# Kernel tuning notes

Hardware: AMD Instinct MI355X
Metric: run time of the kernel (lower is better)

The kernel has to match this reference:

```python
import jax, jax.numpy as jnp
import numpy as np

NUM_HEADS = 16
HEAD_DIM = 256  # hidden_size // num_heads = 4096 // 16
SEQ = 240       # hardcoded in the original forward's view(1, 240, -1)
IN_SIZE = 4096
HID = 4096


def setup_inputs() -> dict:
    key = jax.random.key(0)
    ks = jax.random.split(key, 10)
    s = 0.02
    return {
        "input1": jax.random.normal(ks[0], (SEQ, IN_SIZE), jnp.float32),
        "input2": jax.random.normal(ks[1], (SEQ, IN_SIZE), jnp.float32),
        "Wq": jax.random.normal(ks[2], (HID, IN_SIZE), jnp.float32) * s,
        "bq": jax.random.normal(ks[3], (HID,), jnp.float32) * s,
        "Wk": jax.random.normal(ks[4], (HID, IN_SIZE), jnp.float32) * s,
        "bk": jax.random.normal(ks[5], (HID,), jnp.float32) * s,
        "Wv": jax.random.normal(ks[6], (HID, IN_SIZE), jnp.float32) * s,
        "bv": jax.random.normal(ks[7], (HID,), jnp.float32) * s,
    }


def reference(input1, input2, Wq, bq, Wk, bk, Wv, bv):
    # QKV projections (torch Linear: x @ W^T + b)
    q = input1 @ Wq.T + bq  # [S, HID]
    k = input2 @ Wk.T + bk
    v = input2 @ Wv.T + bv
    # [1, H, S, hd]
    q = q.reshape(1, SEQ, NUM_HEADS, HEAD_DIM).transpose(0, 2, 1, 3)
    k = k.reshape(1, SEQ, NUM_HEADS, HEAD_DIM).transpose(0, 2, 1, 3)
    v = v.reshape(1, SEQ, NUM_HEADS, HEAD_DIM).transpose(0, 2, 1, 3)
    scores = jnp.einsum("bhqd,bhkd->bhqk", q, k) / jnp.sqrt(jnp.float32(HEAD_DIM))
    w = jax.nn.softmax(scores, axis=-1)  # [1, H, Sq, Sk]
    # NOTE: the original does attention_weights.transpose(-2,-1) @ value, i.e. attn^T @ V
    out = jnp.einsum("bhqk,bhqd->bhkd", w, v)  # [1, H, Sk, hd]
    out = out.transpose(0, 2, 1, 3).reshape(1, SEQ, HID)
    # linear_out exists in __init__ but is never applied in forward.
    return out
```

## Files before the change

### kernel.cpp

```cpp
#include <hip/hip_runtime.h>
#include <hip/hip_bf16.h>

#define SEQ 240
#define HID 4096
#define NH 16
#define HD 256

typedef float f32x4 __attribute__((ext_vector_type(4)));
typedef short s16x8 __attribute__((ext_vector_type(8)));
typedef short s16x4 __attribute__((ext_vector_type(4)));

__device__ __forceinline__ short f2bf(float f) {
    unsigned u = __builtin_bit_cast(unsigned, f);
    unsigned r = u + 0x7FFFu + ((u >> 16) & 1u);
    return (short)(r >> 16);
}

__device__ __forceinline__ s16x8 cvt8(float4 a, float4 b) {
    s16x8 r;
    r[0] = f2bf(a.x); r[1] = f2bf(a.y); r[2] = f2bf(a.z); r[3] = f2bf(a.w);
    r[4] = f2bf(b.x); r[5] = f2bf(b.y); r[6] = f2bf(b.z); r[7] = f2bf(b.w);
    return r;
}

__device__ __forceinline__ s16x8 cvt8v(f32x4 a, f32x4 b) {
    s16x8 r;
    r[0] = f2bf(a[0]); r[1] = f2bf(a[1]); r[2] = f2bf(a[2]); r[3] = f2bf(a[3]);
    r[4] = f2bf(b[0]); r[5] = f2bf(b[1]); r[6] = f2bf(b[2]); r[7] = f2bf(b[3]);
    return r;
}

__device__ __forceinline__ void dma16(const void* g, void* l) {
    __builtin_amdgcn_global_load_lds(
        (const __attribute__((address_space(1))) unsigned int*)g,
        (__attribute__((address_space(3))) unsigned int*)l,
        16, 0, 0);
}

__global__ __launch_bounds__(256) void cvt_kernel(
    const float* __restrict__ in1, const float* __restrict__ in2,
    short* __restrict__ A1, short* __restrict__ A2)
{
    const int i = blockIdx.x * 256 + threadIdx.x;
    const float* __restrict__ src = blockIdx.y ? in2 : in1;
    short* __restrict__ dst = blockIdx.y ? A2 : A1;
    const int r = i >> 9;
    const int c = (i & 511) * 8;
    s16x8 v = (s16x8){0,0,0,0,0,0,0,0};
    if (r < SEQ) {
        float4 a = *(const float4*)&src[(size_t)r * HID + c];
        float4 b = *(const float4*)&src[(size_t)r * HID + c + 4];
        v = cvt8(a, b);
    }
    *(s16x8*)&dst[(size_t)r * HID + c] = v;
}

__global__ __launch_bounds__(256, 3) void qkv_gemm(
    const short* __restrict__ A1, const short* __restrict__ A2,
    const float* __restrict__ Wq, const float* __restrict__ Wk,
    const float* __restrict__ Wv,
    float* __restrict__ pqk, float* __restrict__ pvt, int KC)
{
    const int g  = blockIdx.y;
    const int z  = blockIdx.z;
    const int nb = blockIdx.x * 64;
    const short* __restrict__ A = (g == 0) ? A1 : A2;
    const float* __restrict__ W = (g == 0) ? Wq : (g == 1) ? Wk : Wv;

    const int tid  = threadIdx.x;
    const int lane = tid & 63;
    const int w    = tid >> 6;
    const int lr   = lane & 15;
    const int lg   = lane >> 4;

    __shared__ short As[2][256 * 32];
    __shared__ float Bs[2][64 * 32];

    f32x4 acc[4][4];
    #pragma unroll
    for (int m = 0; m < 4; ++m)
        #pragma unroll
        for (int n = 0; n < 4; ++n)
            acc[m][n] = (f32x4){0.f, 0.f, 0.f, 0.f};

    const short* gA[4];
    #pragma unroll
    for (int i = 0; i < 4; ++i) {
        const int row = (i * 4 + w) * 16 + (lane >> 2);
        const int c   = (lane & 3) ^ ((row >> 1) & 3);
        gA[i] = A + (size_t)row * HID + z * KC + c * 8;
    }
    const float* gW[2];
    #pragma unroll
    for (int i = 0; i < 2; ++i) {
        const int row = (i * 4 + w) * 8 + (lane >> 3);
        const int c   = (lane & 7) ^ (row & 7);
        gW[i] = W + (size_t)(nb + row) * HID + z * KC + c * 4;
    }

    int aoff[4];
    #pragma unroll
    for (int m = 0; m < 4; ++m) {
        const int row = w * 64 + m * 16 + lr;
        aoff[m] = row * 32 + ((lg ^ ((row >> 1) & 3)) * 8);
    }
    int boff0[4], boff1[4];
    #pragma unroll
    for (int n = 0; n < 4; ++n) {
        const int row = n * 16 + lr;
        boff0[n] = row * 32 + (((2 * lg)     ^ (row & 7)) * 4);
        boff1[n] = row * 32 + (((2 * lg + 1) ^ (row & 7)) * 4);
    }

    #pragma unroll
    for (int i = 0; i < 4; ++i) dma16(gA[i], &As[0][(i * 4 + w) * 512]);
    #pragma unroll
    for (int i = 0; i < 2; ++i) dma16(gW[i], &Bs[0][(i * 4 + w) * 256]);
    #pragma unroll
    for (int i = 0; i < 4; ++i) gA[i] += 32;
    #pragma unroll
    for (int i = 0; i < 2; ++i) gW[i] += 32;
    __syncthreads();

    const int NIT = KC / 32;
    for (int t = 0; t < NIT; ++t) {
        const int b = t & 1;
        if (t + 1 < NIT) {
            #pragma unroll
            for (int i = 0; i < 4; ++i) dma16(gA[i], &As[b ^ 1][(i * 4 + w) * 512]);
            #pragma unroll
            for (int i = 0; i < 2; ++i) dma16(gW[i], &Bs[b ^ 1][(i * 4 + w) * 256]);
            #pragma unroll
            for (int i = 0; i < 4; ++i) gA[i] += 32;
            #pragma unroll
            for (int i = 0; i < 2; ++i) gW[i] += 32;
        }

        s16x8 af[4], bf[4];
        #pragma unroll
        for (int m = 0; m < 4; ++m)
            af[m] = *(const s16x8*)&As[b][aoff[m]];
        #pragma unroll
        for (int n = 0; n < 4; ++n) {
            f32x4 x0 = *(const f32x4*)&Bs[b][boff0[n]];
            f32x4 x1 = *(const f32x4*)&Bs[b][boff1[n]];
            bf[n] = cvt8v(x0, x1);
        }
        #pragma unroll
        for (int m = 0; m < 4; ++m)
            #pragma unroll
            for (int n = 0; n < 4; ++n)
                acc[m][n] = __builtin_amdgcn_mfma_f32_16x16x32_bf16(af[m], bf[n], acc[m][n], 0, 0, 0);

        if (t + 1 < NIT) __syncthreads();
    }

    if (g == 2) {
        float* pout = pvt + (size_t)z * HID * SEQ;
        #pragma unroll
        for (int m = 0; m < 4; ++m) {
            const int row0 = w * 64 + m * 16 + lg * 4;
            if (row0 >= SEQ) continue;
            #pragma unroll
            for (int n = 0; n < 4; ++n) {
                const int col = nb + n * 16 + lr;
                float4 o = make_float4(acc[m][n][0], acc[m][n][1], acc[m][n][2], acc[m][n][3]);
                *(float4*)&pout[(size_t)col * SEQ + row0] = o;
            }
        }
    } else {
        float* pout = pqk + (size_t)(z * 2 + g) * SEQ * HID;
        #pragma unroll
        for (int m = 0; m < 4; ++m) {
            const int row0 = w * 64 + m * 16 + lg * 4;
            if (row0 >= SEQ) continue;
            #pragma unroll
            for (int n = 0; n < 4; ++n) {
                const int col = nb + n * 16 + lr;
                #pragma unroll
                for (int r = 0; r < 4; ++r)
                    pout[(size_t)(row0 + r) * HID + col] = acc[m][n][r];
            }
        }
    }
}

__global__ __launch_bounds__(256) void reduce_qk(
    const float* __restrict__ pqk,
    const float* __restrict__ bq, const float* __restrict__ bk,
    short* __restrict__ qb, short* __restrict__ kb, int KS)
{
    const int g   = blockIdx.y;
    const int idx = blockIdx.x * 256 + threadIdx.x;
    f32x4 s = (f32x4){0.f, 0.f, 0.f, 0.f};
    for (int z = 0; z < KS; ++z)
        s += *(const f32x4*)&pqk[(size_t)(z * 2 + g) * SEQ * HID + (size_t)idx * 4];
    const int n = (idx * 4) & (HID - 1);
    const float* bias = g ? bk : bq;
    s += *(const f32x4*)&bias[n];
    short* ob = g ? kb : qb;
    s16x4 o = (s16x4){f2bf(s[0]), f2bf(s[1]), f2bf(s[2]), f2bf(s[3])};
    *(s16x4*)&ob[(size_t)idx * 4] = o;
}

__global__ __launch_bounds__(256) void reduce_v(
    const float* __restrict__ pvt, const float* __restrict__ bv,
    short* __restrict__ vtb, int KS)
{
    const int idx = blockIdx.x * 256 + threadIdx.x;
    f32x4 s = (f32x4){0.f, 0.f, 0.f, 0.f};
    for (int z = 0; z < KS; ++z)
        s += *(const f32x4*)&pvt[(size_t)z * HID * SEQ + (size_t)idx * 4];
    const int n = idx / 60;
    const float b = bv[n];
    s16x4 o = (s16x4){f2bf(s[0] + b), f2bf(s[1] + b), f2bf(s[2] + b), f2bf(s[3] + b)};
    *(s16x4*)&vtb[(size_t)idx * 4] = o;
}

__global__ __launch_bounds__(256) void scores_kernel(
    const short* __restrict__ qb, const short* __restrict__ kb,
    short* __restrict__ ptb)
{
    const int it   = blockIdx.x;
    const int h    = blockIdx.y;
    const int tid  = threadIdx.x;
    const int lane = tid & 63;
    const int w    = tid >> 6;
    const int lr   = lane & 15;
    const int lg   = lane >> 4;
    const int jt0  = w * 4;
    const int NJT  = (w < 3) ? 4 : 3;

    __shared__ float redmax[4][16];
    __shared__ float redsum[4][16];

    f32x4 acc[4];
    #pragma unroll
    for (int j = 0; j < 4; ++j) acc[j] = (f32x4){0.f, 0.f, 0.f, 0.f};

    const int ib = it * 16;
    const short* qrow = &qb[(size_t)(ib + lr) * HID + h * HD + lg * 8];

    for (int d0 = 0; d0 < HD; d0 += 32) {
        s16x8 afr = *(const s16x8*)&qrow[d0];
        #pragma unroll
        for (int j = 0; j < 4; ++j) {
            if (j < NJT) {
                s16x8 bfr = *(const s16x8*)&kb[(size_t)((jt0 + j) * 16 + lr) * HID + h * HD + d0 + lg * 8];
                acc[j] = __builtin_amdgcn_mfma_f32_16x16x32_bf16(afr, bfr, acc[j], 0, 0, 0);
            }
        }
    }

    const float sc = 0.0625f;
    #pragma unroll
    for (int j = 0; j < 4; ++j) acc[j] *= sc;

    #pragma unroll
    for (int r = 0; r < 4; ++r) {
        float mx = -1e30f;
        #pragma unroll
        for (int j = 0; j < 4; ++j) if (j < NJT) mx = fmaxf(mx, acc[j][r]);
        #pragma unroll
        for (int s = 1; s < 16; s <<= 1) mx = fmaxf(mx, __shfl_xor(mx, s, 64));
        if (lr == 0) redmax[w][lg * 4 + r] = mx;
    }
    __syncthreads();
    #pragma unroll
    for (int r = 0; r < 4; ++r) {
        const int i = lg * 4 + r;
        float mx = fmaxf(fmaxf(redmax[0][i], redmax[1][i]),
                         fmaxf(redmax[2][i], redmax[3][i]));
        float sum = 0.f;
        #pragma unroll
        for (int j = 0; j < 4; ++j) {
            if (j < NJT) {
                float e = expf(acc[j][r] - mx);
                acc[j][r] = e;
                sum += e;
            }
        }
        #pragma unroll
        for (int s = 1; s < 16; s <<= 1) sum += __shfl_xor(sum, s, 64);
        if (lr == 0) redsum[w][i] = sum;
    }
    __syncthreads();
    #pragma unroll
    for (int r = 0; r < 4; ++r) {
        const int i = lg * 4 + r;
        const float inv = 1.f / (redsum[0][i] + redsum[1][i] + redsum[2][i] + redsum[3][i]);
        #pragma unroll
        for (int j = 0; j < 4; ++j) if (j < NJT) acc[j][r] *= inv;
    }
    #pragma unroll
    for (int j = 0; j < 4; ++j) {
        if (j < NJT) {
            const int jj = (jt0 + j) * 16 + lr;
            s16x4 o = (s16x4){f2bf(acc[j][0]), f2bf(acc[j][1]), f2bf(acc[j][2]), f2bf(acc[j][3])};
            *(s16x4*)&ptb[(size_t)(h * SEQ + jj) * SEQ + ib + lg * 4] = o;
        }
    }
}

__global__ __launch_bounds__(256) void pv_kernel(
    const short* __restrict__ ptb, const short* __restrict__ vtb,
    float* __restrict__ out)
{
    const int dt   = blockIdx.x;
    const int h    = blockIdx.y;
    const int tid  = threadIdx.x;
    const int lane = tid & 63;
    const int w    = tid >> 6;
    const int lr   = lane & 15;
    const int lg   = lane >> 4;
    const int NJT  = (w < 3) ? 4 : 3;

    f32x4 acc[4];
    #pragma unroll
    for (int j = 0; j < 4; ++j) acc[j] = (f32x4){0.f, 0.f, 0.f, 0.f};

    const short* vrow = &vtb[(size_t)(h * HD + dt * 16 + lr) * SEQ + lg * 8];

    for (int i0 = 0; i0 < 256; i0 += 32) {
        const bool ok = (i0 + lg * 8) < SEQ;
        s16x8 bfr = (s16x8){0,0,0,0,0,0,0,0};
        if (ok) bfr = *(const s16x8*)&vrow[i0];
        #pragma unroll
        for (int j = 0; j < 4; ++j) {
            if (j < NJT) {
                const int jt = w + j * 4;
                s16x8 afr = (s16x8){0,0,0,0,0,0,0,0};
                if (ok) afr = *(const s16x8*)&ptb[(size_t)(h * SEQ + jt * 16 + lr) * SEQ + i0 + lg * 8];
                acc[j] = __builtin_amdgcn_mfma_f32_16x16x32_bf16(afr, bfr, acc[j], 0, 0, 0);
            }
        }
    }

    #pragma unroll
    for (int j = 0; j < 4; ++j) {
        if (j < NJT) {
            const int jt = w + j * 4;
            #pragma unroll
            for (int r = 0; r < 4; ++r)
                out[(size_t)(jt * 16 + lg * 4 + r) * HID + h * HD + dt * 16 + lr] = acc[j][r];
        }
    }
}

extern "C" void kernel_launch(void* const* d_in, const int* in_sizes, int n_in,
                              void* d_out, int out_size, void* d_ws, size_t ws_size,
                              hipStream_t stream) {
    const float* in1 = (const float*)d_in[0];
    const float* in2 = (const float*)d_in[1];
    const float* Wq  = (const float*)d_in[2];
    const float* bq  = (const float*)d_in[3];
    const float* Wk  = (const float*)d_in[4];
    const float* bk  = (const float*)d_in[5];
    const float* Wv  = (const float*)d_in[6];
    const float* bv  = (const float*)d_in[7];
    float* out = (float*)d_out;

    char* w = (char*)d_ws;
    short* A1  = (short*)w;  w += (size_t)256 * HID * 2;
    short* A2  = (short*)w;  w += (size_t)256 * HID * 2;
    short* qb  = (short*)w;  w += (size_t)SEQ * HID * 2;
    short* kb  = (short*)w;  w += (size_t)SEQ * HID * 2;
    short* vtb = (short*)w;  w += (size_t)HID * SEQ * 2;
    short* ptb = (short*)w;  w += (size_t)NH * SEQ * SEQ * 2;
    float* pqk = (float*)w;
    const size_t fixed  = (size_t)(w - (char*)d_ws);
    const size_t perKS  = ((size_t)2 * SEQ * HID + (size_t)HID * SEQ) * sizeof(float);

    int KS = 1;
    if (fixed + 4 * perKS <= ws_size)      KS = 4;
    else if (fixed + 2 * perKS <= ws_size) KS = 2;
    const int KC = HID / KS;
    float* pvt = pqk + (size_t)KS * 2 * SEQ * HID;

    cvt_kernel<<<dim3(512, 2), 256, 0, stream>>>(in1, in2, A1, A2);
    qkv_gemm<<<dim3(64, 3, KS), 256, 0, stream>>>(A1, A2, Wq, Wk, Wv, pqk, pvt, KC);
    reduce_qk<<<dim3(960, 2), 256, 0, stream>>>(pqk, bq, bk, qb, kb, KS);
    reduce_v<<<960, 256, 0, stream>>>(pvt, bv, vtb, KS);
    scores_kernel<<<dim3(15, 16), 256, 0, stream>>>(qb, kb, ptb);
    pv_kernel<<<dim3(16, 16), 256, 0, stream>>>(ptb, vtb, out);
}
```

Baseline: 109.9 us.

## Prefetch two stages ahead with explicit vmcnt waits and hardware bf16 pack conversion

```diff
diff --git a/kernel.cpp b/kernel.cpp
--- a/kernel.cpp
+++ b/kernel.cpp
@@ -23,11 +23,13 @@
     return r;
 }
 
-__device__ __forceinline__ s16x8 cvt8v(f32x4 a, f32x4 b) {
-    s16x8 r;
-    r[0] = f2bf(a[0]); r[1] = f2bf(a[1]); r[2] = f2bf(a[2]); r[3] = f2bf(a[3]);
-    r[4] = f2bf(b[0]); r[5] = f2bf(b[1]); r[6] = f2bf(b[2]); r[7] = f2bf(b[3]);
-    return r;
+__device__ __forceinline__ s16x8 cvtpk8(f32x4 a, f32x4 b) {
+    union { unsigned u[4]; s16x8 s; } r;
+    asm("v_cvt_pk_bf16_f32 %0, %1, %2" : "=v"(r.u[0]) : "v"(a[0]), "v"(a[1]));
+    asm("v_cvt_pk_bf16_f32 %0, %1, %2" : "=v"(r.u[1]) : "v"(a[2]), "v"(a[3]));
+    asm("v_cvt_pk_bf16_f32 %0, %1, %2" : "=v"(r.u[2]) : "v"(b[0]), "v"(b[1]));
+    asm("v_cvt_pk_bf16_f32 %0, %1, %2" : "=v"(r.u[3]) : "v"(b[2]), "v"(b[3]));
+    return r.s;
 }
 
 __device__ __forceinline__ void dma16(const void* g, void* l) {
@@ -85,17 +87,17 @@
 
     const short* gA[4];
     #pragma unroll
-    for (int i = 0; i < 4; ++i) {
-        const int row = (i * 4 + w) * 16 + (lane >> 2);
+    for (int j = 0; j < 4; ++j) {
+        const int row = (j * 4 + w) * 16 + (lane >> 2);
         const int c   = (lane & 3) ^ ((row >> 1) & 3);
-        gA[i] = A + (size_t)row * HID + z * KC + c * 8;
+        gA[j] = A + (size_t)row * HID + (size_t)z * KC + c * 8;
     }
     const float* gW[2];
     #pragma unroll
-    for (int i = 0; i < 2; ++i) {
-        const int row = (i * 4 + w) * 8 + (lane >> 3);
+    for (int j = 0; j < 2; ++j) {
+        const int row = (j * 4 + w) * 8 + (lane >> 3);
         const int c   = (lane & 7) ^ (row & 7);
-        gW[i] = W + (size_t)(nb + row) * HID + z * KC + c * 4;
+        gW[j] = W + (size_t)(nb + row) * HID + (size_t)z * KC + c * 4;
     }
 
     int aoff[4];
@@ -112,29 +114,23 @@
         boff1[n] = row * 32 + (((2 * lg + 1) ^ (row & 7)) * 4);
     }
 
-    #pragma unroll
-    for (int i = 0; i < 4; ++i) dma16(gA[i], &As[0][(i * 4 + w) * 512]);
-    #pragma unroll
-    for (int i = 0; i < 2; ++i) dma16(gW[i], &Bs[0][(i * 4 + w) * 256]);
-    #pragma unroll
-    for (int i = 0; i < 4; ++i) gA[i] += 32;
-    #pragma unroll
-    for (int i = 0; i < 2; ++i) gW[i] += 32;
-    __syncthreads();
+#define ISSUE(bb) {                                                          \
+    _Pragma("unroll")                                                        \
+    for (int j = 0; j < 4; ++j) {                                            \
+        dma16(gA[j], &As[bb][(j * 4 + w) * 512]);  gA[j] += 32; }            \
+    _Pragma("unroll")                                                        \
+    for (int j = 0; j < 2; ++j) {                                            \
+        dma16(gW[j], &Bs[bb][(j * 4 + w) * 256]);  gW[j] += 32; } }
+
+    ISSUE(0)
+    ISSUE(1)
+    asm volatile("s_waitcnt vmcnt(6)" ::: "memory");
+    __builtin_amdgcn_s_barrier();
+    __builtin_amdgcn_sched_barrier(0);
 
     const int NIT = KC / 32;
     for (int t = 0; t < NIT; ++t) {
         const int b = t & 1;
-        if (t + 1 < NIT) {
-            #pragma unroll
-            for (int i = 0; i < 4; ++i) dma16(gA[i], &As[b ^ 1][(i * 4 + w) * 512]);
-            #pragma unroll
-            for (int i = 0; i < 2; ++i) dma16(gW[i], &Bs[b ^ 1][(i * 4 + w) * 256]);
-            #pragma unroll
-            for (int i = 0; i < 4; ++i) gA[i] += 32;
-            #pragma unroll
-            for (int i = 0; i < 2; ++i) gW[i] += 32;
-        }
 
         s16x8 af[4], bf[4];
         #pragma unroll
@@ -144,7 +140,7 @@
         for (int n = 0; n < 4; ++n) {
             f32x4 x0 = *(const f32x4*)&Bs[b][boff0[n]];
             f32x4 x1 = *(const f32x4*)&Bs[b][boff1[n]];
-            bf[n] = cvt8v(x0, x1);
+            bf[n] = cvtpk8(x0, x1);
         }
         #pragma unroll
         for (int m = 0; m < 4; ++m)
@@ -152,8 +148,21 @@
             for (int n = 0; n < 4; ++n)
                 acc[m][n] = __builtin_amdgcn_mfma_f32_16x16x32_bf16(af[m], bf[n], acc[m][n], 0, 0, 0);
 
-        if (t + 1 < NIT) __syncthreads();
-    }
+        if (t + 1 < NIT) {
+            asm volatile("s_waitcnt lgkmcnt(0)" ::: "memory");
+            __builtin_amdgcn_s_barrier();
+            __builtin_amdgcn_sched_barrier(0);
+            if (t + 2 < NIT) {
+                ISSUE(b)
+                asm volatile("s_waitcnt vmcnt(6)" ::: "memory");
+            } else {
+                asm volatile("s_waitcnt vmcnt(0)" ::: "memory");
+            }
+            __builtin_amdgcn_s_barrier();
+            __builtin_amdgcn_sched_barrier(0);
+        }
+    }
+#undef ISSUE
 
     if (g == 2) {
         float* pout = pvt + (size_t)z * HID * SEQ;
```

New measurement: 106.5 us. -3.1%, faster.
